# Performance work log

Hardware: AMD Instinct MI355X
Metric: run time of the kernel (lower is better)

The kernel has to match this reference:

```python
import jax, jax.numpy as jnp
import numpy as np

H = 1024
B_DIM = 64  # bottleneck
EPS = 1e-5

def setup_inputs() -> dict:
    key = jax.random.key(0)
    ks = jax.random.split(key, 5)
    x = jax.random.normal(ks[0], (8, 4096, H), dtype=jnp.float32)
    norm_w = jnp.ones((H,), jnp.float32)
    norm_b = jnp.zeros((H,), jnp.float32)
    # nn.Linear default init ~ U(-1/sqrt(fan_in), 1/sqrt(fan_in))
    lim_d = 1.0 / np.sqrt(H)
    down_w = jax.random.uniform(ks[1], (B_DIM, H), jnp.float32, -lim_d, lim_d)
    down_b = jax.random.uniform(ks[2], (B_DIM,), jnp.float32, -lim_d, lim_d)
    # NOTE: original inits up to zeros; we use small random values so the
    # computation (and gradients) are non-degenerate for kernel testing.
    lim_u = 1.0 / np.sqrt(B_DIM)
    up_w = jax.random.uniform(ks[3], (H, B_DIM), jnp.float32, -lim_u, lim_u)
    up_b = jax.random.uniform(ks[4], (H,), jnp.float32, -lim_u, lim_u)
    return {"x": x, "norm_w": norm_w, "norm_b": norm_b,
            "down_w": down_w, "down_b": down_b, "up_w": up_w, "up_b": up_b}

def reference(x, norm_w, norm_b, down_w, down_b, up_w, up_b):
    # LayerNorm over last dim, eps=1e-5 (PyTorch default)
    mu = jnp.mean(x, axis=-1, keepdims=True)
    var = jnp.mean(jnp.square(x - mu), axis=-1, keepdims=True)
    xn = (x - mu) * jax.lax.rsqrt(var + EPS) * norm_w + norm_b
    # down-proj [B,S,H] @ [H,b] -> [B,S,b]
    h = jnp.einsum('bsh,dh->bsd', xn, down_w) + down_b
    h = jax.nn.gelu(h, approximate=False)  # torch nn.GELU default = exact erf
    # up-proj [B,S,b] @ [b,H] -> [B,S,H], residual add
    out = jnp.einsum('bsd,hd->bsh', h, up_w) + up_b
    return x + out
```

## Files before the change

kernel.cpp:

```cpp
#include <hip/hip_runtime.h>


#define HDIM 1024
#define BDIM 64
#define RT   16
#define XPAD 1032
#define GPAD 72

using s16x8 = __attribute__((ext_vector_type(8))) short;
using s16x4 = __attribute__((ext_vector_type(4))) short;
using f32x4 = __attribute__((ext_vector_type(4))) float;

__device__ __forceinline__ short f2bf(float f) {
  unsigned u = __builtin_bit_cast(unsigned, f);
  u += 0x7fffu + ((u >> 16) & 1u);
  return (short)(u >> 16);
}
__device__ __forceinline__ float bf2f(short s) {
  unsigned u = ((unsigned)(unsigned short)s) << 16;
  return __builtin_bit_cast(float, u);
}

extern "C" __global__ __launch_bounds__(256, 2)
void adapter_fused(const float* __restrict__ x,
                   const float* __restrict__ nw, const float* __restrict__ nb,
                   const float* __restrict__ dw, const float* __restrict__ db,
                   const float* __restrict__ uw, const float* __restrict__ ub,
                   float* __restrict__ out)
{
  __shared__ __align__(16) short xbf[RT][XPAD];
  __shared__ __align__(16) short xnbf[RT][XPAD];
  __shared__ __align__(16) short gbf[RT][GPAD];
  __shared__ float wln[HDIM];
  __shared__ float bln[HDIM];

  const int t  = threadIdx.x;
  const int rb = blockIdx.x * RT;

  {
    f32x4 w4 = ((const f32x4*)nw)[t];
    f32x4 b4 = ((const f32x4*)nb)[t];
    *(f32x4*)&wln[t * 4] = w4;
    *(f32x4*)&bln[t * 4] = b4;
  }

  const int r  = t >> 4;
  const int cl = t & 15;
  const float* xrow = x + (size_t)(rb + r) * HDIM;
  float sum = 0.f, ssq = 0.f;
#pragma unroll
  for (int i = 0; i < 16; ++i) {
    int j4 = i * 16 + cl;
    f32x4 v = ((const f32x4*)xrow)[j4];
    s16x4 s;
#pragma unroll
    for (int k = 0; k < 4; ++k) { float f = v[k]; sum += f; ssq += f * f; s[k] = f2bf(f); }
    *(s16x4*)&xbf[r][j4 * 4] = s;
  }
#pragma unroll
  for (int m = 1; m < 16; m <<= 1) {
    sum += __shfl_xor(sum, m, 64);
    ssq += __shfl_xor(ssq, m, 64);
  }
  const float mu = sum * (1.0f / HDIM);
  const float var = ssq * (1.0f / HDIM) - mu * mu;
  const float rs = rsqrtf(var + 1e-5f);
  __syncthreads();

#pragma unroll
  for (int i = 0; i < 16; ++i) {
    int j = (i * 16 + cl) * 4;
    s16x4 s = *(const s16x4*)&xbf[r][j];
    s16x4 o;
#pragma unroll
    for (int k = 0; k < 4; ++k) {
      float xf = bf2f(s[k]);
      o[k] = f2bf((xf - mu) * rs * wln[j + k] + bln[j + k]);
    }
    *(s16x4*)&xnbf[r][j] = o;
  }
  __syncthreads();

  const int wv   = t >> 6;
  const int lane = t & 63;
  const int q    = lane >> 4;
  const int c    = lane & 15;
  f32x4 acc = {0.f, 0.f, 0.f, 0.f};
  const float* dwrow = dw + (size_t)(wv * 16 + c) * HDIM;
#pragma unroll 4
  for (int ks = 0; ks < 32; ++ks) {
    int k0 = ks * 32 + q * 8;
    s16x8 a = *(const s16x8*)&xnbf[c][k0];
    f32x4 b0 = *(const f32x4*)(dwrow + k0);
    f32x4 b1 = *(const f32x4*)(dwrow + k0 + 4);
    s16x8 b;
#pragma unroll
    for (int k = 0; k < 4; ++k) { b[k] = f2bf(b0[k]); b[k + 4] = f2bf(b1[k]); }
    acc = __builtin_amdgcn_mfma_f32_16x16x32_bf16(a, b, acc, 0, 0, 0);
  }

  {
    float dbv = db[wv * 16 + c];
#pragma unroll
    for (int i = 0; i < 4; ++i) {
      float hv = acc[i] + dbv;
      float g  = 0.5f * hv * (1.0f + erff(hv * 0.70710678118654752f));
      gbf[q * 4 + i][wv * 16 + c] = f2bf(g);
    }
  }
  __syncthreads();

  s16x8 a0 = *(const s16x8*)&gbf[c][q * 8];
  s16x8 a1 = *(const s16x8*)&gbf[c][32 + q * 8];
#pragma unroll 2
  for (int nt = 0; nt < 16; ++nt) {
    int ncol = wv * 256 + nt * 16 + c;
    const float* uwrow = uw + (size_t)ncol * BDIM;
    f32x4 u0 = *(const f32x4*)(uwrow + q * 8);
    f32x4 u1 = *(const f32x4*)(uwrow + q * 8 + 4);
    f32x4 u2 = *(const f32x4*)(uwrow + 32 + q * 8);
    f32x4 u3 = *(const f32x4*)(uwrow + 32 + q * 8 + 4);
    s16x8 b0, b1;
#pragma unroll
    for (int k = 0; k < 4; ++k) {
      b0[k] = f2bf(u0[k]); b0[k + 4] = f2bf(u1[k]);
      b1[k] = f2bf(u2[k]); b1[k + 4] = f2bf(u3[k]);
    }
    f32x4 o4 = {0.f, 0.f, 0.f, 0.f};
    o4 = __builtin_amdgcn_mfma_f32_16x16x32_bf16(a0, b0, o4, 0, 0, 0);
    o4 = __builtin_amdgcn_mfma_f32_16x16x32_bf16(a1, b1, o4, 0, 0, 0);
    float ubv = ub[ncol];
#pragma unroll
    for (int i = 0; i < 4; ++i) {
      int row = q * 4 + i;
      float xres = bf2f(xbf[row][ncol]);
      out[(size_t)(rb + row) * HDIM + ncol] = o4[i] + ubv + xres;
    }
  }
}

extern "C" void kernel_launch(void* const* d_in, const int* in_sizes, int n_in,
                              void* d_out, int out_size, void* d_ws, size_t ws_size,
                              hipStream_t stream) {
  const float* x  = (const float*)d_in[0];
  const float* nw = (const float*)d_in[1];
  const float* nb = (const float*)d_in[2];
  const float* dw = (const float*)d_in[3];
  const float* db = (const float*)d_in[4];
  const float* uw = (const float*)d_in[5];
  const float* ub = (const float*)d_in[6];
  float* out = (float*)d_out;

  const int rows = in_sizes[0] / HDIM;
  const int grid = rows / RT;
  adapter_fused<<<grid, 256, 0, stream>>>(x, nw, nb, dw, db, uw, ub, out);
}
```

Measured before the change: 331.2 us.

## Pre-convert weights to bf16 and process 32 rows per 512-thread block

```diff
diff --git a/kernel.cpp b/kernel.cpp
--- a/kernel.cpp
+++ b/kernel.cpp
@@ -3,13 +3,14 @@
 
 #define HDIM 1024
 #define BDIM 64
-#define RT   16
+#define RT   32
 #define XPAD 1032
 #define GPAD 72
 
 using s16x8 = __attribute__((ext_vector_type(8))) short;
 using s16x4 = __attribute__((ext_vector_type(4))) short;
 using f32x4 = __attribute__((ext_vector_type(4))) float;
+using f32x2 = __attribute__((ext_vector_type(2))) float;
 
 __device__ __forceinline__ short f2bf(float f) {
   unsigned u = __builtin_bit_cast(unsigned, f);
@@ -21,14 +22,27 @@
   return __builtin_bit_cast(float, u);
 }
 
-extern "C" __global__ __launch_bounds__(256, 2)
+extern "C" __global__ void prep_weights(const float* __restrict__ dw,
+                                        const float* __restrict__ uw,
+                                        short* __restrict__ wsbf) {
+  int tid = blockIdx.x * 256 + threadIdx.x;
+  const float* src = (tid < 8192) ? dw : uw;
+  int off = (tid < 8192) ? tid * 8 : (tid - 8192) * 8;
+  f32x4 v0 = *(const f32x4*)(src + off);
+  f32x4 v1 = *(const f32x4*)(src + off + 4);
+  s16x8 o;
+#pragma unroll
+  for (int k = 0; k < 4; ++k) { o[k] = f2bf(v0[k]); o[k + 4] = f2bf(v1[k]); }
+  *(s16x8*)(wsbf + tid * 8) = o;
+}
+
+extern "C" __global__ __launch_bounds__(512, 4)
 void adapter_fused(const float* __restrict__ x,
                    const float* __restrict__ nw, const float* __restrict__ nb,
-                   const float* __restrict__ dw, const float* __restrict__ db,
-                   const float* __restrict__ uw, const float* __restrict__ ub,
+                   const float* __restrict__ db, const float* __restrict__ ub,
+                   const short* __restrict__ dwb, const short* __restrict__ uwb,
                    float* __restrict__ out)
 {
-  __shared__ __align__(16) short xbf[RT][XPAD];
   __shared__ __align__(16) short xnbf[RT][XPAD];
   __shared__ __align__(16) short gbf[RT][GPAD];
   __shared__ float wln[HDIM];
@@ -38,39 +52,38 @@
   const int rb = blockIdx.x * RT;
 
   {
-    f32x4 w4 = ((const f32x4*)nw)[t];
-    f32x4 b4 = ((const f32x4*)nb)[t];
-    *(f32x4*)&wln[t * 4] = w4;
-    *(f32x4*)&bln[t * 4] = b4;
+    f32x2 w2 = ((const f32x2*)nw)[t];
+    f32x2 b2 = ((const f32x2*)nb)[t];
+    *(f32x2*)&wln[t * 2] = w2;
+    *(f32x2*)&bln[t * 2] = b2;
   }
 
   const int r  = t >> 4;
   const int cl = t & 15;
   const float* xrow = x + (size_t)(rb + r) * HDIM;
   float sum = 0.f, ssq = 0.f;
-#pragma unroll
+#pragma unroll 8
   for (int i = 0; i < 16; ++i) {
     int j4 = i * 16 + cl;
     f32x4 v = ((const f32x4*)xrow)[j4];
     s16x4 s;
 #pragma unroll
     for (int k = 0; k < 4; ++k) { float f = v[k]; sum += f; ssq += f * f; s[k] = f2bf(f); }
-    *(s16x4*)&xbf[r][j4 * 4] = s;
+    *(s16x4*)&xnbf[r][j4 * 4] = s;
   }
 #pragma unroll
   for (int m = 1; m < 16; m <<= 1) {
-    sum += __shfl_xor(sum, m, 64);
-    ssq += __shfl_xor(ssq, m, 64);
+    sum += __shfl_xor(sum, m);
+    ssq += __shfl_xor(ssq, m);
   }
-  const float mu = sum * (1.0f / HDIM);
+  const float mu  = sum * (1.0f / HDIM);
   const float var = ssq * (1.0f / HDIM) - mu * mu;
-  const float rs = rsqrtf(var + 1e-5f);
-  __syncthreads();
+  const float rs  = rsqrtf(var + 1e-5f);
 
 #pragma unroll
   for (int i = 0; i < 16; ++i) {
     int j = (i * 16 + cl) * 4;
-    s16x4 s = *(const s16x4*)&xbf[r][j];
+    s16x4 s = *(const s16x4*)&xnbf[r][j];
     s16x4 o;
 #pragma unroll
     for (int k = 0; k < 4; ++k) {
@@ -81,60 +94,51 @@
   }
   __syncthreads();
 
-  const int wv   = t >> 6;
+  const int w    = t >> 6;
   const int lane = t & 63;
   const int q    = lane >> 4;
   const int c    = lane & 15;
+  const int rt   = w & 1;
+  const int ct   = w >> 1;
   f32x4 acc = {0.f, 0.f, 0.f, 0.f};
-  const float* dwrow = dw + (size_t)(wv * 16 + c) * HDIM;
+  const short* dwrow = dwb + (size_t)(ct * 16 + c) * HDIM;
 #pragma unroll 4
   for (int ks = 0; ks < 32; ++ks) {
     int k0 = ks * 32 + q * 8;
-    s16x8 a = *(const s16x8*)&xnbf[c][k0];
-    f32x4 b0 = *(const f32x4*)(dwrow + k0);
-    f32x4 b1 = *(const f32x4*)(dwrow + k0 + 4);
-    s16x8 b;
-#pragma unroll
-    for (int k = 0; k < 4; ++k) { b[k] = f2bf(b0[k]); b[k + 4] = f2bf(b1[k]); }
+    s16x8 a = *(const s16x8*)&xnbf[rt * 16 + c][k0];
+    s16x8 b = *(const s16x8*)(dwrow + k0);
     acc = __builtin_amdgcn_mfma_f32_16x16x32_bf16(a, b, acc, 0, 0, 0);
   }
 
   {
-    float dbv = db[wv * 16 + c];
+    float dbv = db[ct * 16 + c];
 #pragma unroll
     for (int i = 0; i < 4; ++i) {
       float hv = acc[i] + dbv;
       float g  = 0.5f * hv * (1.0f + erff(hv * 0.70710678118654752f));
-      gbf[q * 4 + i][wv * 16 + c] = f2bf(g);
+      gbf[rt * 16 + q * 4 + i][ct * 16 + c] = f2bf(g);
     }
   }
   __syncthreads();
 
-  s16x8 a0 = *(const s16x8*)&gbf[c][q * 8];
-  s16x8 a1 = *(const s16x8*)&gbf[c][32 + q * 8];
+  s16x8 a0 = *(const s16x8*)&gbf[rt * 16 + c][q * 8];
+  s16x8 a1 = *(const s16x8*)&gbf[rt * 16 + c][32 + q * 8];
+  const float* xbase = x   + (size_t)(rb + rt * 16) * HDIM;
+  float*       obase = out + (size_t)(rb + rt * 16) * HDIM;
 #pragma unroll 2
   for (int nt = 0; nt < 16; ++nt) {
-    int ncol = wv * 256 + nt * 16 + c;
-    const float* uwrow = uw + (size_t)ncol * BDIM;
-    f32x4 u0 = *(const f32x4*)(uwrow + q * 8);
-    f32x4 u1 = *(const f32x4*)(uwrow + q * 8 + 4);
-    f32x4 u2 = *(const f32x4*)(uwrow + 32 + q * 8);
-    f32x4 u3 = *(const f32x4*)(uwrow + 32 + q * 8 + 4);
-    s16x8 b0, b1;
-#pragma unroll
-    for (int k = 0; k < 4; ++k) {
-      b0[k] = f2bf(u0[k]); b0[k + 4] = f2bf(u1[k]);
-      b1[k] = f2bf(u2[k]); b1[k + 4] = f2bf(u3[k]);
-    }
+    int ncol = ct * 256 + nt * 16 + c;
+    const short* uwrow = uwb + (size_t)ncol * BDIM;
+    s16x8 b0 = *(const s16x8*)(uwrow + q * 8);
+    s16x8 b1 = *(const s16x8*)(uwrow + 32 + q * 8);
     f32x4 o4 = {0.f, 0.f, 0.f, 0.f};
     o4 = __builtin_amdgcn_mfma_f32_16x16x32_bf16(a0, b0, o4, 0, 0, 0);
     o4 = __builtin_amdgcn_mfma_f32_16x16x32_bf16(a1, b1, o4, 0, 0, 0);
     float ubv = ub[ncol];
 #pragma unroll
     for (int i = 0; i < 4; ++i) {
-      int row = q * 4 + i;
-      float xres = bf2f(xbf[row][ncol]);
-      out[(size_t)(rb + row) * HDIM + ncol] = o4[i] + ubv + xres;
+      int ro = (q * 4 + i) * HDIM + ncol;
+      obase[ro] = o4[i] + ubv + xbase[ro];
     }
   }
 }
@@ -151,7 +155,11 @@
   const float* ub = (const float*)d_in[6];
   float* out = (float*)d_out;
 
+  short* wsbf = (short*)d_ws;
+  prep_weights<<<64, 256, 0, stream>>>(dw, uw, wsbf);
+
   const int rows = in_sizes[0] / HDIM;
   const int grid = rows / RT;
-  adapter_fused<<<grid, 256, 0, stream>>>(x, nw, nb, dw, db, uw, ub, out);
+  adapter_fused<<<grid, 512, 0, stream>>>(x, nw, nb, db, ub,
+                                          wsbf, wsbf + 65536, out);
 }
```

Result: faster. 290.1 us (-12.4%).
